# Performance work log

Hardware: AMD Instinct MI355X
Metric: run time of the kernel (lower is better)

The kernel has to match this reference:

```python
import jax, jax.numpy as jnp
import numpy as np

N = 50000          # nb_nodes
DEG = 32           # avg degree -> every node has DEG outgoing edges (rows covered)
E = N * DEG        # 1,600,000 edges
F_IN = 512
F_OUT = 256


def setup_inputs() -> dict:
    key = jax.random.key(0)
    k = jax.random.split(key, 8)
    x = jax.random.normal(k[0], (1, N, F_IN), dtype=jnp.float32)
    W = jax.random.normal(k[1], (F_IN, F_OUT), dtype=jnp.float32) * 0.05
    a1_w = jax.random.normal(k[2], (F_OUT, 1), dtype=jnp.float32) * 0.05
    a1_b = jnp.zeros((1,), jnp.float32)
    a2_w = jax.random.normal(k[3], (F_OUT, 1), dtype=jnp.float32) * 0.05
    a2_b = jnp.zeros((1,), jnp.float32)
    bias_out = jnp.zeros((F_OUT,), jnp.float32)
    # edge list: each node has exactly DEG neighbors (rows sorted, all rows present)
    edge_row = jnp.repeat(jnp.arange(N, dtype=jnp.int32), DEG)
    edge_col = jax.random.randint(k[4], (E,), 0, N, dtype=jnp.int32)
    bias_vals = jnp.ones((E,), jnp.float32)  # SparseTensor values of bias_mat
    return {"x": x, "W": W, "a1_w": a1_w, "a1_b": a1_b, "a2_w": a2_w,
            "a2_b": a2_b, "bias_out": bias_out, "bias_vals": bias_vals,
            "edge_row": edge_row, "edge_col": edge_col}


def reference(x, W, a1_w, a1_b, a2_w, a2_b, bias_out, bias_vals, edge_row, edge_col):
    # conv1d(k=1, no bias): per-node linear projection. x: [1, N, F_IN]
    seq = jnp.einsum('nf,fo->no', x[0], W)                 # [N, F_OUT]
    f1 = (seq @ a1_w + a1_b)[:, 0]                         # [N]
    f2 = (seq @ a2_w + a2_b)[:, 0]                         # [N]
    # sparse_add(bias_mat*f1_row, bias_mat^T-style*f2_col) -> per-edge logits
    e = bias_vals * f1[edge_row] + bias_vals * f2[edge_col]  # [E]
    e = jax.nn.leaky_relu(e, negative_slope=0.2)
    # sparse_softmax: softmax over nonzero entries of each row
    row_max = jax.ops.segment_max(e, edge_row, num_segments=N)
    row_max = jnp.where(jnp.isfinite(row_max), row_max, 0.0)
    ee = jnp.exp(e - row_max[edge_row])
    denom = jax.ops.segment_sum(ee, edge_row, num_segments=N)
    coefs = ee / jnp.maximum(denom[edge_row], 1e-30)        # [E]
    # SpMM: out[i] = sum_j coefs[ij] * seq[j]
    vals = jax.ops.segment_sum(coefs[:, None] * seq[edge_col], edge_row,
                               num_segments=N)             # [N, F_OUT]
    ret = jax.nn.elu(vals + bias_out)[None]                # [1, N, F_OUT]
    return ret
```

## Files before the change

kernel.cpp:

```cpp
#include <hip/hip_runtime.h>
#include <stdint.h>

#define N_NODES 50000
#define DEG 32
#define FIN 512
#define FOUT 256

typedef __attribute__((ext_vector_type(4))) float f32x4;
typedef __attribute__((ext_vector_type(8))) short short8;

__device__ __forceinline__ unsigned short f2bf(float f) {
    union { float f; unsigned int u; } v; v.f = f;
    unsigned int u = v.u;
    return (unsigned short)((u + 0x7FFFu + ((u >> 16) & 1u)) >> 16);
}

__device__ __forceinline__ void gll16(const void* g, void* l) {
    __builtin_amdgcn_global_load_lds(
        (const __attribute__((address_space(1))) unsigned int*)g,
        (__attribute__((address_space(3))) unsigned int*)(uintptr_t)l,
        16, 0, 0);
}

__global__ void k_wt(const float* __restrict__ W, unsigned short* __restrict__ Wt) {
    int idx = blockIdx.x * 256 + threadIdx.x;
    int c = idx >> 9;
    int k = idx & 511;
    Wt[idx] = f2bf(W[k * FOUT + c]);
}

#define GBM 64
#define GBK 64

__global__ __launch_bounds__(512, 2)
void k_gemm(const float* __restrict__ x, const unsigned short* __restrict__ Wt,
            const float* __restrict__ a1w, const float* __restrict__ a1b,
            const float* __restrict__ a2w, const float* __restrict__ a2b,
            float* __restrict__ f1, float* __restrict__ f2,
            float* __restrict__ scale, unsigned int* __restrict__ seq8) {
    __shared__ unsigned short As[2][8 * 512];
    __shared__ unsigned short Bs[2][32 * 512];

    const int tid  = threadIdx.x;
    const int lane = tid & 63;
    const int w    = tid >> 6;
    const int row0 = blockIdx.x * GBM;
    const int fr   = lane & 15;
    const int fq   = lane >> 4;

    const int af = w >> 1, as_ = w & 1;
    int arow = row0 + af * 16 + fr;
    if (arow >= N_NODES) arow = N_NODES - 1;
    const float* aptr = x + (size_t)arow * FIN + as_ * 32 + fq * 8;
    const int awoff = (w << 9) + lane * 8;

    const unsigned short* bsrc[4];
    int boff[4];
#pragma unroll
    for (int c = 0; c < 4; c++) {
        int frag = w * 4 + c;
        int n16 = frag >> 1, bs_ = frag & 1;
        bsrc[c] = Wt + (size_t)(n16 * 16 + fr) * FIN + bs_ * 32 + fq * 8;
        boff[c] = frag << 9;
    }

    const int mf0 = (w >> 2) * 2;
    const int nc0 = (w & 3) * 4;
    const int mg = w >> 2, ng = w & 3;
    const int n0 = ng * 64;

    f32x4 acc[2][4];
    f32x4 zero4 = {0.f, 0.f, 0.f, 0.f};
#pragma unroll
    for (int i = 0; i < 2; i++)
#pragma unroll
        for (int j = 0; j < 4; j++) acc[i][j] = zero4;

#pragma unroll
    for (int c = 0; c < 4; c++) gll16(bsrc[c], &Bs[0][boff[c]]);
    {
        float4 p0 = *(const float4*)(aptr);
        float4 p1 = *(const float4*)(aptr + 4);
        ushort4 lo = { f2bf(p0.x), f2bf(p0.y), f2bf(p0.z), f2bf(p0.w) };
        ushort4 hi = { f2bf(p1.x), f2bf(p1.y), f2bf(p1.z), f2bf(p1.w) };
        *(ushort4*)&As[0][awoff]     = lo;
        *(ushort4*)&As[0][awoff + 4] = hi;
    }
    __syncthreads();

    for (int t = 0; t < 8; ++t) {
        const int rb = t & 1, wb = rb ^ 1;
        float4 q0, q1;
        if (t < 7) {
            int kk = (t + 1) * GBK;
#pragma unroll
            for (int c = 0; c < 4; c++) gll16(bsrc[c] + kk, &Bs[wb][boff[c]]);
            q0 = *(const float4*)(aptr + kk);
            q1 = *(const float4*)(aptr + kk + 4);
        }
#pragma unroll
        for (int s = 0; s < 2; ++s) {
            short8 a0 = *(const short8*)(const void*)&As[rb][((mf0 + 0) * 2 + s) * 512 + lane * 8];
            short8 a1 = *(const short8*)(const void*)&As[rb][((mf0 + 1) * 2 + s) * 512 + lane * 8];
            short8 b0 = *(const short8*)(const void*)&Bs[rb][((nc0 + 0) * 2 + s) * 512 + lane * 8];
            short8 b1 = *(const short8*)(const void*)&Bs[rb][((nc0 + 1) * 2 + s) * 512 + lane * 8];
            short8 b2 = *(const short8*)(const void*)&Bs[rb][((nc0 + 2) * 2 + s) * 512 + lane * 8];
            short8 b3 = *(const short8*)(const void*)&Bs[rb][((nc0 + 3) * 2 + s) * 512 + lane * 8];
            acc[0][0] = __builtin_amdgcn_mfma_f32_16x16x32_bf16(a0, b0, acc[0][0], 0, 0, 0);
            acc[0][1] = __builtin_amdgcn_mfma_f32_16x16x32_bf16(a0, b1, acc[0][1], 0, 0, 0);
            acc[0][2] = __builtin_amdgcn_mfma_f32_16x16x32_bf16(a0, b2, acc[0][2], 0, 0, 0);
            acc[0][3] = __builtin_amdgcn_mfma_f32_16x16x32_bf16(a0, b3, acc[0][3], 0, 0, 0);
            acc[1][0] = __builtin_amdgcn_mfma_f32_16x16x32_bf16(a1, b0, acc[1][0], 0, 0, 0);
            acc[1][1] = __builtin_amdgcn_mfma_f32_16x16x32_bf16(a1, b1, acc[1][1], 0, 0, 0);
            acc[1][2] = __builtin_amdgcn_mfma_f32_16x16x32_bf16(a1, b2, acc[1][2], 0, 0, 0);
            acc[1][3] = __builtin_amdgcn_mfma_f32_16x16x32_bf16(a1, b3, acc[1][3], 0, 0, 0);
        }
        if (t < 7) {
            ushort4 lo = { f2bf(q0.x), f2bf(q0.y), f2bf(q0.z), f2bf(q0.w) };
            ushort4 hi = { f2bf(q1.x), f2bf(q1.y), f2bf(q1.z), f2bf(q1.w) };
            *(ushort4*)&As[wb][awoff]     = lo;
            *(ushort4*)&As[wb][awoff + 4] = hi;
            __syncthreads();
        }
    }

    __syncthreads();
    float* f1p_l  = (float*)(void*)As;
    float* f2p_l  = f1p_l + 256;
    float* am_l   = f2p_l + 256;
    float* finv_l = am_l + 256;

    const float w10 = a1w[n0 + fr],      w11 = a1w[n0 + 16 + fr];
    const float w12 = a1w[n0 + 32 + fr], w13 = a1w[n0 + 48 + fr];
    const float w20 = a2w[n0 + fr],      w21 = a2w[n0 + 16 + fr];
    const float w22 = a2w[n0 + 32 + fr], w23 = a2w[n0 + 48 + fr];

#pragma unroll
    for (int mi = 0; mi < 2; mi++) {
#pragma unroll
        for (int r = 0; r < 4; r++) {
            float c0 = acc[mi][0][r], c1 = acc[mi][1][r];
            float c2 = acc[mi][2][r], c3 = acc[mi][3][r];
            float s1 = c0 * w10 + c1 * w11 + c2 * w12 + c3 * w13;
            float s2 = c0 * w20 + c1 * w21 + c2 * w22 + c3 * w23;
            float am = fmaxf(fmaxf(fabsf(c0), fabsf(c1)),
                             fmaxf(fabsf(c2), fabsf(c3)));
#pragma unroll
            for (int off = 1; off < 16; off <<= 1) {
                s1 += __shfl_xor(s1, off, 64);
                s2 += __shfl_xor(s2, off, 64);
                am = fmaxf(am, __shfl_xor(am, off, 64));
            }
            if (fr == 0) {
                int rowb = mg * 32 + mi * 16 + fq * 4 + r;
                f1p_l[rowb * 4 + ng] = s1;
                f2p_l[rowb * 4 + ng] = s2;
                am_l[rowb * 4 + ng]  = am;
            }
        }
    }
    __syncthreads();

    if (tid < 64) {
        float4 p1 = *(const float4*)&f1p_l[tid * 4];
        float4 p2 = *(const float4*)&f2p_l[tid * 4];
        float4 pm = *(const float4*)&am_l[tid * 4];
        float s1 = p1.x + p1.y + p1.z + p1.w + a1b[0];
        float s2 = p2.x + p2.y + p2.z + p2.w + a2b[0];
        float am = fmaxf(fmaxf(pm.x, pm.y), fmaxf(pm.z, pm.w));
        am = fmaxf(am, 1e-8f);
        int grow = row0 + tid;
        if (grow < N_NODES) {
            f1[grow] = s1;
            f2[grow] = s2;
            scale[grow] = am * (1.0f / 127.0f);
        }
        finv_l[tid] = 127.0f / am;
    }
    __syncthreads();

#pragma unroll
    for (int mi = 0; mi < 2; mi++) {
#pragma unroll
        for (int r = 0; r < 4; r++) {
            int rowb = mg * 32 + mi * 16 + fq * 4 + r;
            int grow = row0 + rowb;
            float inv = finv_l[rowb];
            int q0 = ((int)rintf(acc[mi][0][r] * inv)) & 255;
            int q1 = ((int)rintf(acc[mi][1][r] * inv)) & 255;
            int q2 = ((int)rintf(acc[mi][2][r] * inv)) & 255;
            int q3 = ((int)rintf(acc[mi][3][r] * inv)) & 255;
            unsigned int pk = (unsigned int)q0 | ((unsigned int)q1 << 8) |
                              ((unsigned int)q2 << 16) | ((unsigned int)q3 << 24);
            if (grow < N_NODES)
                seq8[(size_t)grow * 64 + ng * 16 + fr] = pk;
        }
    }
}

#define LOADS(J) \
    int   c##J = __shfl(col,  (J), 64); \
    float w##J = __shfl(coef, (J), 64); \
    int   v##J = *(const int*)(const void*)(sp + (size_t)c##J * FOUT);

#define ACCUM(J) \
    a0 += w##J * (float)((v##J << 24) >> 24); \
    a1 += w##J * (float)((v##J << 16) >> 24); \
    a2 += w##J * (float)((v##J <<  8) >> 24); \
    a3 += w##J * (float)( v##J        >> 24);

__global__ __launch_bounds__(256, 4)
void k_attn(const char* __restrict__ seq8, const float* __restrict__ scale,
            const float* __restrict__ f1, const float* __restrict__ f2,
            const float* __restrict__ bias_vals,
            const int* __restrict__ edge_col,
            const float* __restrict__ bias_out,
            float* __restrict__ out) {
    const int lane = threadIdx.x & 63;
    const int node = (blockIdx.x * 256 + threadIdx.x) >> 6;

    float e = -1e30f;
    int col = 0;
    float sc = 0.f;
    if (lane < 32) {
        int eidx = node * DEG + lane;
        col = edge_col[eidx];
        sc  = scale[col];
        float bv = bias_vals[eidx];
        e = bv * f1[node] + bv * f2[col];
        e = (e >= 0.f) ? e : 0.2f * e;
    }
    float m = e;
#pragma unroll
    for (int off = 16; off; off >>= 1) m = fmaxf(m, __shfl_xor(m, off, 32));
    float p = __expf(e - m);
    float s = p;
#pragma unroll
    for (int off = 16; off; off >>= 1) s += __shfl_xor(s, off, 32);
    float coef = (p / s) * sc;

    const char* sp = seq8 + lane * 4;
    float a0 = 0.f, a1 = 0.f, a2 = 0.f, a3 = 0.f;
    {
        LOADS(0) LOADS(1) LOADS(2) LOADS(3) LOADS(4) LOADS(5) LOADS(6) LOADS(7)
        ACCUM(0) ACCUM(1) ACCUM(2) ACCUM(3) ACCUM(4) ACCUM(5) ACCUM(6) ACCUM(7)
    }
    {
        LOADS(8) LOADS(9) LOADS(10) LOADS(11) LOADS(12) LOADS(13) LOADS(14) LOADS(15)
        ACCUM(8) ACCUM(9) ACCUM(10) ACCUM(11) ACCUM(12) ACCUM(13) ACCUM(14) ACCUM(15)
    }
    {
        LOADS(16) LOADS(17) LOADS(18) LOADS(19) LOADS(20) LOADS(21) LOADS(22) LOADS(23)
        ACCUM(16) ACCUM(17) ACCUM(18) ACCUM(19) ACCUM(20) ACCUM(21) ACCUM(22) ACCUM(23)
    }
    {
        LOADS(24) LOADS(25) LOADS(26) LOADS(27) LOADS(28) LOADS(29) LOADS(30) LOADS(31)
        ACCUM(24) ACCUM(25) ACCUM(26) ACCUM(27) ACCUM(28) ACCUM(29) ACCUM(30) ACCUM(31)
    }

    const int fb = (lane >> 4) * 64 + (lane & 15);
    float b0 = bias_out[fb], b1 = bias_out[fb + 16];
    float b2 = bias_out[fb + 32], b3 = bias_out[fb + 48];
    float r0 = a0 + b0, r1 = a1 + b1, r2 = a2 + b2, r3 = a3 + b3;
    r0 = (r0 > 0.f) ? r0 : expm1f(r0);
    r1 = (r1 > 0.f) ? r1 : expm1f(r1);
    r2 = (r2 > 0.f) ? r2 : expm1f(r2);
    r3 = (r3 > 0.f) ? r3 : expm1f(r3);
    float* op = out + (size_t)node * FOUT + fb;
    op[0]  = r0;
    op[16] = r1;
    op[32] = r2;
    op[48] = r3;
}

extern "C" void kernel_launch(void* const* d_in, const int* in_sizes, int n_in,
                              void* d_out, int out_size, void* d_ws, size_t ws_size,
                              hipStream_t stream) {
    const float* x         = (const float*)d_in[0];
    const float* W         = (const float*)d_in[1];
    const float* a1w       = (const float*)d_in[2];
    const float* a1b       = (const float*)d_in[3];
    const float* a2w       = (const float*)d_in[4];
    const float* a2b       = (const float*)d_in[5];
    const float* bias_out  = (const float*)d_in[6];
    const float* bias_vals = (const float*)d_in[7];
    const int* edge_col    = (const int*)d_in[9];
    float* out = (float*)d_out;

    char* ws = (char*)d_ws;
    unsigned short* Wt = (unsigned short*)ws;
    float* f1    = (float*)(ws + 262144);
    float* f2    = (float*)(ws + 262144 + 200064);
    float* scale = (float*)(ws + 262144 + 2 * 200064);
    unsigned int* seq8 = (unsigned int*)(ws + 262144 + 3 * 200064);

    hipLaunchKernelGGL(k_wt,   dim3(512), dim3(256), 0, stream, W, Wt);
    hipLaunchKernelGGL(k_gemm, dim3((N_NODES + GBM - 1) / GBM), dim3(512), 0, stream,
                       x, Wt, a1w, a1b, a2w, a2b, f1, f2, scale, seq8);
    hipLaunchKernelGGL(k_attn, dim3(N_NODES / 4), dim3(256), 0, stream,
                       (const char*)seq8, scale, f1, f2, bias_vals, edge_col,
                       bias_out, out);
}
```

Before: 117.8 us.

## Stage full A tile in LDS once and stream W fragments from global

Replaces the double-buffered K-loop, which staged both the x tile and the transposed weight tile through LDS, with a single up-front load of the whole 64x512 x tile as bf16 into LDS. The MFMA loop then reads B fragments directly from global memory, where they should mostly hit cache because every block reads the same small weight matrix. Launch bounds rise to 4 blocks per CU, which the smaller LDS footprint allows. In exchange there is no overlap between the x load and the MFMAs, each B fragment is fetched from global memory by every block instead of once per tile, and register pressure may be tighter.

```diff
diff --git a/kernel.cpp b/kernel.cpp
--- a/kernel.cpp
+++ b/kernel.cpp
@@ -13,13 +13,6 @@
     union { float f; unsigned int u; } v; v.f = f;
     unsigned int u = v.u;
     return (unsigned short)((u + 0x7FFFu + ((u >> 16) & 1u)) >> 16);
-}
-
-__device__ __forceinline__ void gll16(const void* g, void* l) {
-    __builtin_amdgcn_global_load_lds(
-        (const __attribute__((address_space(1))) unsigned int*)g,
-        (__attribute__((address_space(3))) unsigned int*)(uintptr_t)l,
-        16, 0, 0);
 }
 
 __global__ void k_wt(const float* __restrict__ W, unsigned short* __restrict__ Wt) {
@@ -30,16 +23,14 @@
 }
 
 #define GBM 64
-#define GBK 64
-
-__global__ __launch_bounds__(512, 2)
+
+__global__ __launch_bounds__(512, 4)
 void k_gemm(const float* __restrict__ x, const unsigned short* __restrict__ Wt,
             const float* __restrict__ a1w, const float* __restrict__ a1b,
             const float* __restrict__ a2w, const float* __restrict__ a2b,
             float* __restrict__ f1, float* __restrict__ f2,
             float* __restrict__ scale, unsigned int* __restrict__ seq8) {
-    __shared__ unsigned short As[2][8 * 512];
-    __shared__ unsigned short Bs[2][32 * 512];
+    __shared__ unsigned short As[64 * 512];
 
     const int tid  = threadIdx.x;
     const int lane = tid & 63;
@@ -47,28 +38,32 @@
     const int row0 = blockIdx.x * GBM;
     const int fr   = lane & 15;
     const int fq   = lane >> 4;
-
-    const int af = w >> 1, as_ = w & 1;
-    int arow = row0 + af * 16 + fr;
-    if (arow >= N_NODES) arow = N_NODES - 1;
-    const float* aptr = x + (size_t)arow * FIN + as_ * 32 + fq * 8;
-    const int awoff = (w << 9) + lane * 8;
-
-    const unsigned short* bsrc[4];
-    int boff[4];
-#pragma unroll
-    for (int c = 0; c < 4; c++) {
-        int frag = w * 4 + c;
-        int n16 = frag >> 1, bs_ = frag & 1;
-        bsrc[c] = Wt + (size_t)(n16 * 16 + fr) * FIN + bs_ * 32 + fq * 8;
-        boff[c] = frag << 9;
-    }
-
-    const int mf0 = (w >> 2) * 2;
-    const int nc0 = (w & 3) * 4;
     const int mg = w >> 2, ng = w & 3;
     const int n0 = ng * 64;
 
+    {
+        int row = lane;
+        int grow = row0 + row; if (grow >= N_NODES) grow = N_NODES - 1;
+        const float* xr = x + (size_t)grow * FIN;
+        int chunkf = (row >> 4) * 16;
+        int rofs = (row & 15) * 8;
+#pragma unroll
+        for (int it = 0; it < 8; ++it) {
+            int kseg = it * 8 + w;
+            int k0 = kseg * 8;
+            float4 a0 = *(const float4*)(xr + k0);
+            float4 a1 = *(const float4*)(xr + k0 + 4);
+            short8 pk;
+            pk[0] = (short)f2bf(a0.x); pk[1] = (short)f2bf(a0.y);
+            pk[2] = (short)f2bf(a0.z); pk[3] = (short)f2bf(a0.w);
+            pk[4] = (short)f2bf(a1.x); pk[5] = (short)f2bf(a1.y);
+            pk[6] = (short)f2bf(a1.z); pk[7] = (short)f2bf(a1.w);
+            int chunk = chunkf + (k0 >> 5);
+            *(short8*)(void*)&As[chunk * 512 + ((k0 >> 3) & 3) * 128 + rofs] = pk;
+        }
+    }
+    __syncthreads();
+
     f32x4 acc[2][4];
     f32x4 zero4 = {0.f, 0.f, 0.f, 0.f};
 #pragma unroll
@@ -76,52 +71,29 @@
 #pragma unroll
         for (int j = 0; j < 4; j++) acc[i][j] = zero4;
 
-#pragma unroll
-    for (int c = 0; c < 4; c++) gll16(bsrc[c], &Bs[0][boff[c]]);
-    {
-        float4 p0 = *(const float4*)(aptr);
-        float4 p1 = *(const float4*)(aptr + 4);
-        ushort4 lo = { f2bf(p0.x), f2bf(p0.y), f2bf(p0.z), f2bf(p0.w) };
-        ushort4 hi = { f2bf(p1.x), f2bf(p1.y), f2bf(p1.z), f2bf(p1.w) };
-        *(ushort4*)&As[0][awoff]     = lo;
-        *(ushort4*)&As[0][awoff + 4] = hi;
-    }
-    __syncthreads();
-
-    for (int t = 0; t < 8; ++t) {
-        const int rb = t & 1, wb = rb ^ 1;
-        float4 q0, q1;
-        if (t < 7) {
-            int kk = (t + 1) * GBK;
-#pragma unroll
-            for (int c = 0; c < 4; c++) gll16(bsrc[c] + kk, &Bs[wb][boff[c]]);
-            q0 = *(const float4*)(aptr + kk);
-            q1 = *(const float4*)(aptr + kk + 4);
-        }
-#pragma unroll
-        for (int s = 0; s < 2; ++s) {
-            short8 a0 = *(const short8*)(const void*)&As[rb][((mf0 + 0) * 2 + s) * 512 + lane * 8];
-            short8 a1 = *(const short8*)(const void*)&As[rb][((mf0 + 1) * 2 + s) * 512 + lane * 8];
-            short8 b0 = *(const short8*)(const void*)&Bs[rb][((nc0 + 0) * 2 + s) * 512 + lane * 8];
-            short8 b1 = *(const short8*)(const void*)&Bs[rb][((nc0 + 1) * 2 + s) * 512 + lane * 8];
-            short8 b2 = *(const short8*)(const void*)&Bs[rb][((nc0 + 2) * 2 + s) * 512 + lane * 8];
-            short8 b3 = *(const short8*)(const void*)&Bs[rb][((nc0 + 3) * 2 + s) * 512 + lane * 8];
-            acc[0][0] = __builtin_amdgcn_mfma_f32_16x16x32_bf16(a0, b0, acc[0][0], 0, 0, 0);
-            acc[0][1] = __builtin_amdgcn_mfma_f32_16x16x32_bf16(a0, b1, acc[0][1], 0, 0, 0);
-            acc[0][2] = __builtin_amdgcn_mfma_f32_16x16x32_bf16(a0, b2, acc[0][2], 0, 0, 0);
-            acc[0][3] = __builtin_amdgcn_mfma_f32_16x16x32_bf16(a0, b3, acc[0][3], 0, 0, 0);
-            acc[1][0] = __builtin_amdgcn_mfma_f32_16x16x32_bf16(a1, b0, acc[1][0], 0, 0, 0);
-            acc[1][1] = __builtin_amdgcn_mfma_f32_16x16x32_bf16(a1, b1, acc[1][1], 0, 0, 0);
-            acc[1][2] = __builtin_amdgcn_mfma_f32_16x16x32_bf16(a1, b2, acc[1][2], 0, 0, 0);
-            acc[1][3] = __builtin_amdgcn_mfma_f32_16x16x32_bf16(a1, b3, acc[1][3], 0, 0, 0);
-        }
-        if (t < 7) {
-            ushort4 lo = { f2bf(q0.x), f2bf(q0.y), f2bf(q0.z), f2bf(q0.w) };
-            ushort4 hi = { f2bf(q1.x), f2bf(q1.y), f2bf(q1.z), f2bf(q1.w) };
-            *(ushort4*)&As[wb][awoff]     = lo;
-            *(ushort4*)&As[wb][awoff + 4] = hi;
-            __syncthreads();
-        }
+    const unsigned short* bp0 = Wt + (size_t)(n0 + 0  + fr) * FIN + fq * 8;
+    const unsigned short* bp1 = Wt + (size_t)(n0 + 16 + fr) * FIN + fq * 8;
+    const unsigned short* bp2 = Wt + (size_t)(n0 + 32 + fr) * FIN + fq * 8;
+    const unsigned short* bp3 = Wt + (size_t)(n0 + 48 + fr) * FIN + fq * 8;
+    const int a0base = ((mg * 2 + 0) * 16) * 512 + lane * 8;
+    const int a1base = ((mg * 2 + 1) * 16) * 512 + lane * 8;
+
+#pragma unroll
+    for (int t = 0; t < 16; ++t) {
+        short8 b0 = *(const short8*)(const void*)(bp0 + t * 32);
+        short8 b1 = *(const short8*)(const void*)(bp1 + t * 32);
+        short8 b2 = *(const short8*)(const void*)(bp2 + t * 32);
+        short8 b3 = *(const short8*)(const void*)(bp3 + t * 32);
+        short8 a0 = *(const short8*)(const void*)&As[a0base + t * 512];
+        short8 a1 = *(const short8*)(const void*)&As[a1base + t * 512];
+        acc[0][0] = __builtin_amdgcn_mfma_f32_16x16x32_bf16(a0, b0, acc[0][0], 0, 0, 0);
+        acc[0][1] = __builtin_amdgcn_mfma_f32_16x16x32_bf16(a0, b1, acc[0][1], 0, 0, 0);
+        acc[0][2] = __builtin_amdgcn_mfma_f32_16x16x32_bf16(a0, b2, acc[0][2], 0, 0, 0);
+        acc[0][3] = __builtin_amdgcn_mfma_f32_16x16x32_bf16(a0, b3, acc[0][3], 0, 0, 0);
+        acc[1][0] = __builtin_amdgcn_mfma_f32_16x16x32_bf16(a1, b0, acc[1][0], 0, 0, 0);
+        acc[1][1] = __builtin_amdgcn_mfma_f32_16x16x32_bf16(a1, b1, acc[1][1], 0, 0, 0);
+        acc[1][2] = __builtin_amdgcn_mfma_f32_16x16x32_bf16(a1, b2, acc[1][2], 0, 0, 0);
+        acc[1][3] = __builtin_amdgcn_mfma_f32_16x16x32_bf16(a1, b3, acc[1][3], 0, 0, 0);
     }
 
     __syncthreads();
```

Result: slower. 145.8 us (+23.7%).

## Pre-tile W into MFMA fragment order and coalesce swizzled A staging

Applied to the files above, without the earlier changes.

The weight transpose kernel now writes bf16 W directly in per-k-tile MFMA fragment order, so each B fragment load in the GEMM is a contiguous 16-byte-per-lane global-to-LDS copy. The A tile loads now have 8 lanes reading consecutive 32-byte chunks of one x row, which coalesces the global reads. Writes into LDS use an XOR swizzle that the fragment reads undo, to avoid bank conflicts. The cost is more complex index arithmetic and a dependence on the swizzle mapping being correct.

```diff
diff --git a/kernel.cpp b/kernel.cpp
--- a/kernel.cpp
+++ b/kernel.cpp
@@ -22,18 +22,22 @@
         16, 0, 0);
 }
 
-__global__ void k_wt(const float* __restrict__ W, unsigned short* __restrict__ Wt) {
+__global__ void k_wt2(const float* __restrict__ W, unsigned short* __restrict__ Wt2) {
     int idx = blockIdx.x * 256 + threadIdx.x;
-    int c = idx >> 9;
-    int k = idx & 511;
-    Wt[idx] = f2bf(W[k * FOUT + c]);
+    int e    = idx & 7;
+    int j    = (idx >> 3) & 63;
+    int frag = (idx >> 9) & 31;
+    int t    = idx >> 14;
+    int n = (frag >> 1) * 16 + (j & 15);
+    int k = t * 64 + (frag & 1) * 32 + (j >> 4) * 8 + e;
+    Wt2[idx] = f2bf(W[k * FOUT + n]);
 }
 
 #define GBM 64
 #define GBK 64
 
 __global__ __launch_bounds__(512, 2)
-void k_gemm(const float* __restrict__ x, const unsigned short* __restrict__ Wt,
+void k_gemm(const float* __restrict__ x, const unsigned short* __restrict__ Wt2,
             const float* __restrict__ a1w, const float* __restrict__ a1b,
             const float* __restrict__ a2w, const float* __restrict__ a2b,
             float* __restrict__ f1, float* __restrict__ f2,
@@ -47,28 +51,30 @@
     const int row0 = blockIdx.x * GBM;
     const int fr   = lane & 15;
     const int fq   = lane >> 4;
-
-    const int af = w >> 1, as_ = w & 1;
-    int arow = row0 + af * 16 + fr;
-    if (arow >= N_NODES) arow = N_NODES - 1;
-    const float* aptr = x + (size_t)arow * FIN + as_ * 32 + fq * 8;
-    const int awoff = (w << 9) + lane * 8;
-
-    const unsigned short* bsrc[4];
-    int boff[4];
-#pragma unroll
-    for (int c = 0; c < 4; c++) {
-        int frag = w * 4 + c;
-        int n16 = frag >> 1, bs_ = frag & 1;
-        bsrc[c] = Wt + (size_t)(n16 * 16 + fr) * FIN + bs_ * 32 + fq * 8;
-        boff[c] = frag << 9;
-    }
-
-    const int mf0 = (w >> 2) * 2;
-    const int nc0 = (w & 3) * 4;
     const int mg = w >> 2, ng = w & 3;
     const int n0 = ng * 64;
 
+    const int r_ = lane >> 3, q_ = lane & 7;
+    int arow = row0 + w * 8 + r_;
+    if (arow >= N_NODES) arow = N_NODES - 1;
+    const float* aptr = x + (size_t)arow * FIN + q_ * 8;
+    const int rowlow = (w & 1) * 8 + r_;
+    const int awoff = ((((w >> 1) * 2 + (q_ >> 2)) << 9)
+                       + ((((q_ & 3) << 4) | (rowlow ^ (q_ & 3))) << 3));
+
+    const unsigned short* bsrc0 = Wt2 + ((w * 4 + 0) << 9) + lane * 8;
+    const unsigned short* bsrc1 = Wt2 + ((w * 4 + 1) << 9) + lane * 8;
+    const unsigned short* bsrc2 = Wt2 + ((w * 4 + 2) << 9) + lane * 8;
+    const unsigned short* bsrc3 = Wt2 + ((w * 4 + 3) << 9) + lane * 8;
+    const int bo0 = ((w * 4 + 0) << 9) + lane * 8;
+    const int bo1 = ((w * 4 + 1) << 9) + lane * 8;
+    const int bo2 = ((w * 4 + 2) << 9) + lane * 8;
+    const int bo3 = ((w * 4 + 3) << 9) + lane * 8;
+
+    const int mf0 = mg * 2;
+    const int nc0 = ng * 4;
+    const int axr = ((fq << 4) | (fr ^ fq)) << 3;
+
     f32x4 acc[2][4];
     f32x4 zero4 = {0.f, 0.f, 0.f, 0.f};
 #pragma unroll
@@ -76,36 +82,44 @@
 #pragma unroll
         for (int j = 0; j < 4; j++) acc[i][j] = zero4;
 
-#pragma unroll
-    for (int c = 0; c < 4; c++) gll16(bsrc[c], &Bs[0][boff[c]]);
-    {
-        float4 p0 = *(const float4*)(aptr);
-        float4 p1 = *(const float4*)(aptr + 4);
-        ushort4 lo = { f2bf(p0.x), f2bf(p0.y), f2bf(p0.z), f2bf(p0.w) };
-        ushort4 hi = { f2bf(p1.x), f2bf(p1.y), f2bf(p1.z), f2bf(p1.w) };
-        *(ushort4*)&As[0][awoff]     = lo;
-        *(ushort4*)&As[0][awoff + 4] = hi;
-    }
+    float4 sa0, sa1;
+#define STAGE_A_LOAD(T) \
+    sa0 = *(const float4*)(aptr + (T) * GBK); \
+    sa1 = *(const float4*)(aptr + (T) * GBK + 4);
+#define STAGE_A_WRITE(BUF) \
+    { short8 pk; \
+      pk[0] = (short)f2bf(sa0.x); pk[1] = (short)f2bf(sa0.y); \
+      pk[2] = (short)f2bf(sa0.z); pk[3] = (short)f2bf(sa0.w); \
+      pk[4] = (short)f2bf(sa1.x); pk[5] = (short)f2bf(sa1.y); \
+      pk[6] = (short)f2bf(sa1.z); pk[7] = (short)f2bf(sa1.w); \
+      *(short8*)(void*)&As[BUF][awoff] = pk; }
+
+    gll16(bsrc0, &Bs[0][bo0]);
+    gll16(bsrc1, &Bs[0][bo1]);
+    gll16(bsrc2, &Bs[0][bo2]);
+    gll16(bsrc3, &Bs[0][bo3]);
+    STAGE_A_LOAD(0)
+    STAGE_A_WRITE(0)
     __syncthreads();
 
     for (int t = 0; t < 8; ++t) {
         const int rb = t & 1, wb = rb ^ 1;
-        float4 q0, q1;
         if (t < 7) {
-            int kk = (t + 1) * GBK;
-#pragma unroll
-            for (int c = 0; c < 4; c++) gll16(bsrc[c] + kk, &Bs[wb][boff[c]]);
-            q0 = *(const float4*)(aptr + kk);
-            q1 = *(const float4*)(aptr + kk + 4);
+            const int ko = (t + 1) * 16384;
+            gll16(bsrc0 + ko, &Bs[wb][bo0]);
+            gll16(bsrc1 + ko, &Bs[wb][bo1]);
+            gll16(bsrc2 + ko, &Bs[wb][bo2]);
+            gll16(bsrc3 + ko, &Bs[wb][bo3]);
+            STAGE_A_LOAD(t + 1)
         }
 #pragma unroll
         for (int s = 0; s < 2; ++s) {
-            short8 a0 = *(const short8*)(const void*)&As[rb][((mf0 + 0) * 2 + s) * 512 + lane * 8];
-            short8 a1 = *(const short8*)(const void*)&As[rb][((mf0 + 1) * 2 + s) * 512 + lane * 8];
-            short8 b0 = *(const short8*)(const void*)&Bs[rb][((nc0 + 0) * 2 + s) * 512 + lane * 8];
-            short8 b1 = *(const short8*)(const void*)&Bs[rb][((nc0 + 1) * 2 + s) * 512 + lane * 8];
-            short8 b2 = *(const short8*)(const void*)&Bs[rb][((nc0 + 2) * 2 + s) * 512 + lane * 8];
-            short8 b3 = *(const short8*)(const void*)&Bs[rb][((nc0 + 3) * 2 + s) * 512 + lane * 8];
+            short8 a0 = *(const short8*)(const void*)&As[rb][(((mf0 + 0) * 2 + s) << 9) + axr];
+            short8 a1 = *(const short8*)(const void*)&As[rb][(((mf0 + 1) * 2 + s) << 9) + axr];
+            short8 b0 = *(const short8*)(const void*)&Bs[rb][(((nc0 + 0) * 2 + s) << 9) + lane * 8];
+            short8 b1 = *(const short8*)(const void*)&Bs[rb][(((nc0 + 1) * 2 + s) << 9) + lane * 8];
+            short8 b2 = *(const short8*)(const void*)&Bs[rb][(((nc0 + 2) * 2 + s) << 9) + lane * 8];
+            short8 b3 = *(const short8*)(const void*)&Bs[rb][(((nc0 + 3) * 2 + s) << 9) + lane * 8];
             acc[0][0] = __builtin_amdgcn_mfma_f32_16x16x32_bf16(a0, b0, acc[0][0], 0, 0, 0);
             acc[0][1] = __builtin_amdgcn_mfma_f32_16x16x32_bf16(a0, b1, acc[0][1], 0, 0, 0);
             acc[0][2] = __builtin_amdgcn_mfma_f32_16x16x32_bf16(a0, b2, acc[0][2], 0, 0, 0);
@@ -116,10 +130,7 @@
             acc[1][3] = __builtin_amdgcn_mfma_f32_16x16x32_bf16(a1, b3, acc[1][3], 0, 0, 0);
         }
         if (t < 7) {
-            ushort4 lo = { f2bf(q0.x), f2bf(q0.y), f2bf(q0.z), f2bf(q0.w) };
-            ushort4 hi = { f2bf(q1.x), f2bf(q1.y), f2bf(q1.z), f2bf(q1.w) };
-            *(ushort4*)&As[wb][awoff]     = lo;
-            *(ushort4*)&As[wb][awoff + 4] = hi;
+            STAGE_A_WRITE(wb)
             __syncthreads();
         }
     }
@@ -288,15 +299,15 @@
     float* out = (float*)d_out;
 
     char* ws = (char*)d_ws;
-    unsigned short* Wt = (unsigned short*)ws;
+    unsigned short* Wt2 = (unsigned short*)ws;
     float* f1    = (float*)(ws + 262144);
     float* f2    = (float*)(ws + 262144 + 200064);
     float* scale = (float*)(ws + 262144 + 2 * 200064);
     unsigned int* seq8 = (unsigned int*)(ws + 262144 + 3 * 200064);
 
-    hipLaunchKernelGGL(k_wt,   dim3(512), dim3(256), 0, stream, W, Wt);
+    hipLaunchKernelGGL(k_wt2, dim3(512), dim3(256), 0, stream, W, Wt2);
     hipLaunchKernelGGL(k_gemm, dim3((N_NODES + GBM - 1) / GBM), dim3(512), 0, stream,
-                       x, Wt, a1w, a1b, a2w, a2b, f1, f2, scale, seq8);
+                       x, Wt2, a1w, a1b, a2w, a2b, f1, f2, scale, seq8);
     hipLaunchKernelGGL(k_attn, dim3(N_NODES / 4), dim3(256), 0, stream,
                        (const char*)seq8, scale, f1, f2, bias_vals, edge_col,
                        bias_out, out);
```

Measured after the change: 102.1 us. 1.15x faster.
